# Kernel optimization log

Measured on AMD Instinct MI355X. Metric: run time of the kernel, lower is better.

The kernel has to match this reference:

```python
import jax, jax.numpy as jnp
import numpy as np

D_MODEL = 1024
N_HEADS = 16
HEAD_DIM = D_MODEL // N_HEADS


def setup_inputs() -> dict:
    key = jax.random.key(0)
    ks = jax.random.split(key, 5)
    s = 0.02  # small init scale to keep softmax numerics reasonable
    x = jax.random.normal(ks[0], (4, 2048, D_MODEL), dtype=jnp.float32)
    w_qkv = jax.random.normal(ks[1], (D_MODEL, 3 * D_MODEL), dtype=jnp.float32) * s
    b_qkv = jnp.zeros((3 * D_MODEL,), dtype=jnp.float32)
    w_proj = jax.random.normal(ks[2], (D_MODEL, D_MODEL), dtype=jnp.float32) * s
    b_proj = jnp.zeros((D_MODEL,), dtype=jnp.float32)
    return {"x": x, "w_qkv": w_qkv, "b_qkv": b_qkv, "w_proj": w_proj, "b_proj": b_proj}


def reference(x, w_qkv, b_qkv, w_proj, b_proj):
    B, T, C = x.shape
    scale = 1.0 / np.sqrt(HEAD_DIM)
    qkv = x @ w_qkv + b_qkv                               # [B,T,3C]
    qkv = qkv.reshape(B, T, 3, N_HEADS, HEAD_DIM)
    q = qkv[:, :, 0].transpose(0, 2, 1, 3)               # [B,H,T,D]
    k = qkv[:, :, 1].transpose(0, 2, 1, 3)
    v = qkv[:, :, 2].transpose(0, 2, 1, 3)
    att = jnp.einsum('bhqd,bhkd->bhqk', q, k) * scale    # [B,H,T,T]
    causal = jnp.tril(jnp.ones((T, T), dtype=bool))
    att = jnp.where(causal, att, -jnp.inf)
    att = jax.nn.softmax(att, axis=-1)
    y = jnp.einsum('bhqk,bhkd->bhqd', att, v)            # [B,H,T,D]
    y = y.transpose(0, 2, 1, 3).reshape(B, T, C)
    y = y @ w_proj + b_proj
    return y
```

## Files before the change

### kernel.cpp

```cpp
#include <hip/hip_runtime.h>
#include <stdint.h>

#define BATCH 4
#define SEQ 2048
#define DMODEL 1024
#define NHEADS 16
#define HDIM 64
#define MROWS (BATCH * SEQ)

typedef float floatx4 __attribute__((ext_vector_type(4)));
typedef __bf16 bf16x8 __attribute__((ext_vector_type(8)));
typedef __bf16 bf16x4 __attribute__((ext_vector_type(4)));
typedef short short8 __attribute__((ext_vector_type(8)));

__device__ __forceinline__ unsigned short f32_to_bf16(float f) {
    union { float f; unsigned int u; } c; c.f = f;
    unsigned int u = c.u;
    unsigned int r = (u + 0x7FFFu + ((u >> 16) & 1u)) >> 16;
    return (unsigned short)r;
}

__device__ __forceinline__ void async_ld16(const void* g, void* l) {
    __builtin_amdgcn_global_load_lds(
        (const __attribute__((address_space(1))) unsigned int*)g,
        (__attribute__((address_space(3))) unsigned int*)l, 16, 0, 0);
}

__global__ __launch_bounds__(256) void conv_f32_bf16(
    const float* __restrict__ in, unsigned short* __restrict__ out, int n4) {
    int i = blockIdx.x * 256 + threadIdx.x;
    if (i < n4) {
        float4 v = ((const float4*)in)[i];
        ushort4 o;
        o.x = f32_to_bf16(v.x); o.y = f32_to_bf16(v.y);
        o.z = f32_to_bf16(v.z); o.w = f32_to_bf16(v.w);
        ((ushort4*)out)[i] = o;
    }
}

__global__ __launch_bounds__(256) void transp_conv(
    const float* __restrict__ in, unsigned short* __restrict__ out, int K, int N) {
    __shared__ float tile[32][33];
    int bx = blockIdx.x * 32;
    int by = blockIdx.y * 32;
    int tx = threadIdx.x, ty = threadIdx.y;
#pragma unroll
    for (int i = 0; i < 4; ++i)
        tile[ty + i * 8][tx] = in[(size_t)(by + ty + i * 8) * N + bx + tx];
    __syncthreads();
#pragma unroll
    for (int i = 0; i < 4; ++i)
        out[(size_t)(bx + ty + i * 8) * K + by + tx] = f32_to_bf16(tile[tx][ty + i * 8]);
}

__global__ __launch_bounds__(256) void transp_bf16_head(
    const unsigned short* __restrict__ in, unsigned short* __restrict__ out) {
    __shared__ unsigned short tile[32][33];
    const unsigned short* src = in + (size_t)blockIdx.z * SEQ * HDIM;
    unsigned short* dst = out + (size_t)blockIdx.z * SEQ * HDIM;
    int bx = blockIdx.x * 32;
    int by = blockIdx.y * 32;
    int tx = threadIdx.x, ty = threadIdx.y;
#pragma unroll
    for (int i = 0; i < 4; ++i)
        tile[ty + i * 8][tx] = src[(size_t)(by + ty + i * 8) * HDIM + bx + tx];
    __syncthreads();
#pragma unroll
    for (int i = 0; i < 4; ++i) {
        int keyg = by + tx;
        int col2 = (keyg & ~63) | (((keyg & 15) << 2) | ((keyg >> 4) & 3));
        dst[(size_t)(bx + ty + i * 8) * SEQ + col2] = tile[tx][ty + i * 8];
    }
}

template <int EPI>
__global__ __launch_bounds__(256, 3) void gemm_bt(
    const unsigned short* __restrict__ A, const unsigned short* __restrict__ Bt,
    const float* __restrict__ bias, float* __restrict__ Cout,
    unsigned short* __restrict__ Qo, unsigned short* __restrict__ Ko,
    unsigned short* __restrict__ Vo, int M, int N, int K) {
    __shared__ __align__(16) unsigned short As[3][128 * 32];
    __shared__ __align__(16) unsigned short Bs[3][128 * 32];
    const int tid = threadIdx.x;
    const int lane = tid & 63;
    const int w = tid >> 6;
    const int wm = w & 1, wn = w >> 1;
    const int quad = lane >> 4, l16 = lane & 15;
    const int m0 = blockIdx.y * 128;
    const int n0 = blockIdx.x * 128;
    const int fsw = (l16 >> 1) & 3;

    const int idx0 = tid, idx1 = tid + 256;
    const int row0 = idx0 >> 2, row1 = idx1 >> 2;
    const int cg0 = (idx0 & 3) ^ ((row0 >> 1) & 3);
    const int cg1 = (idx1 & 3) ^ ((row1 >> 1) & 3);
    const unsigned short* Ar0 = &A[(size_t)(m0 + row0) * K + cg0 * 8];
    const unsigned short* Ar1 = &A[(size_t)(m0 + row1) * K + cg1 * 8];
    const unsigned short* Br0 = &Bt[(size_t)(n0 + row0) * K + cg0 * 8];
    const unsigned short* Br1 = &Bt[(size_t)(n0 + row1) * K + cg1 * 8];

    floatx4 acc[4][4];
#pragma unroll
    for (int mt = 0; mt < 4; ++mt)
#pragma unroll
        for (int nt = 0; nt < 4; ++nt) acc[mt][nt] = (floatx4){0.f, 0.f, 0.f, 0.f};

    async_ld16(Ar0, &As[0][idx0 * 8]);
    async_ld16(Br0, &Bs[0][idx0 * 8]);
    async_ld16(Ar1, &As[0][idx1 * 8]);
    async_ld16(Br1, &Bs[0][idx1 * 8]);
    async_ld16(Ar0 + 32, &As[1][idx0 * 8]);
    async_ld16(Br0 + 32, &Bs[1][idx0 * 8]);
    async_ld16(Ar1 + 32, &As[1][idx1 * 8]);
    async_ld16(Br1 + 32, &Bs[1][idx1 * 8]);

    const int nk = K >> 5;
    int bcur = 0, bpre = 2;
    for (int kt = 0; kt < nk; ++kt) {
        if (kt + 2 < nk)
            asm volatile("s_waitcnt vmcnt(4)" ::: "memory");
        else
            asm volatile("s_waitcnt vmcnt(0)" ::: "memory");
        __builtin_amdgcn_s_barrier();
        asm volatile("" ::: "memory");

        if (kt + 2 < nk) {
            const int ko = (kt + 2) << 5;
            async_ld16(Ar0 + ko, &As[bpre][idx0 * 8]);
            async_ld16(Br0 + ko, &Bs[bpre][idx0 * 8]);
            async_ld16(Ar1 + ko, &As[bpre][idx1 * 8]);
            async_ld16(Br1 + ko, &Bs[bpre][idx1 * 8]);
        }

        bf16x8 aF[4], bF[4];
#pragma unroll
        for (int mt = 0; mt < 4; ++mt)
            aF[mt] = *(const bf16x8*)&As[bcur][(wm * 64 + mt * 16 + l16) * 32 + (quad ^ fsw) * 8];
#pragma unroll
        for (int nt = 0; nt < 4; ++nt)
            bF[nt] = *(const bf16x8*)&Bs[bcur][(wn * 64 + nt * 16 + l16) * 32 + (quad ^ fsw) * 8];
#pragma unroll
        for (int mt = 0; mt < 4; ++mt)
#pragma unroll
            for (int nt = 0; nt < 4; ++nt)
                acc[mt][nt] = __builtin_amdgcn_mfma_f32_16x16x32_bf16(
                    aF[mt], bF[nt], acc[mt][nt], 0, 0, 0);

        bcur = (bcur == 2) ? 0 : bcur + 1;
        bpre = (bpre == 2) ? 0 : bpre + 1;
    }

#pragma unroll
    for (int mt = 0; mt < 4; ++mt)
#pragma unroll
        for (int nt = 0; nt < 4; ++nt)
#pragma unroll
            for (int r = 0; r < 4; ++r) {
                int m = m0 + wm * 64 + mt * 16 + quad * 4 + r;
                int n = n0 + wn * 64 + nt * 16 + l16;
                float v = acc[mt][nt][r] + bias[n];
                if (EPI == 1) {
                    Cout[(size_t)m * N + n] = v;
                } else {
                    int sel = n >> 10, c = n & 1023;
                    int head = c >> 6, d = c & 63;
                    int bb = m >> 11, t = m & 2047;
                    unsigned short* dst = sel == 0 ? Qo : (sel == 1 ? Ko : Vo);
                    dst[((((size_t)bb * NHEADS + head) * SEQ + t) << 6) + d] = f32_to_bf16(v);
                }
            }
}

__global__ __launch_bounds__(256, 2) void attn_kernel(
    const unsigned short* __restrict__ Qg, const unsigned short* __restrict__ Kg,
    const unsigned short* __restrict__ Vtg, unsigned short* __restrict__ Yatt) {
    __shared__ __align__(16) unsigned short Kb2[2][4096];
    __shared__ __align__(16) unsigned short Vb2[2][4096];
    __shared__ __align__(16) unsigned short Ps[4][2048];

    const int tid = threadIdx.x;
    const int lane = tid & 63;
    const int w = tid >> 6;
    const int quad = lane >> 4, l16 = lane & 15;
    const int bh = blockIdx.x;
    const int by = blockIdx.y;
    const int sA = by * 4 + w;
    const size_t base = (size_t)bh * SEQ * HDIM;
    const int bIdx = bh >> 4, h = bh & 15;
    unsigned short* Pw = &Ps[w][0];
    const float csc = 0.18033688f;

    const int lrow = lane >> 3;
    const int lch = (lane & 7) ^ lrow;

    short8 osv = {0x3F80, 0x3F80, 0x3F80, 0x3F80, 0x3F80, 0x3F80, 0x3F80, 0x3F80};
    bf16x8 ones = __builtin_bit_cast(bf16x8, osv);

    for (int half = 0; half < 2; ++half) {
        const int rowb = (half == 0 ? sA : 63 - sA) * 32;
        const int kmaxB = (half == 0) ? (2 * by + 2) : (32 - 2 * by);

        bf16x8 qf[2][2];
#pragma unroll
        for (int mt = 0; mt < 2; ++mt)
#pragma unroll
            for (int kk = 0; kk < 2; ++kk)
                qf[mt][kk] = *(const bf16x8*)&Qg[base + (size_t)(rowb + mt * 16 + l16) * 64 +
                                                 kk * 32 + quad * 8];

        floatx4 lsum[2];
        floatx4 o[2][4];
#pragma unroll
        for (int mt = 0; mt < 2; ++mt) {
            lsum[mt] = (floatx4){0.f, 0.f, 0.f, 0.f};
#pragma unroll
            for (int nt = 0; nt < 4; ++nt) o[mt][nt] = (floatx4){0.f, 0.f, 0.f, 0.f};
        }

        {
            const unsigned short* Ktg = Kg + base;
            const unsigned short* Vtg_t = Vtg + base;
#pragma unroll
            for (int ii = 0; ii < 2; ++ii) {
                int i = w * 2 + ii;
                async_ld16(Ktg + (i * 8 + lrow) * 64 + lch * 8,
                           &Kb2[0][i * 512 + lane * 8]);
                async_ld16(Vtg_t + (size_t)(i * 8 + lrow) * SEQ + lch * 8,
                           &Vb2[0][i * 512 + lane * 8]);
            }
        }

        for (int kb = 0; kb < kmaxB; ++kb) {
            const int b = kb & 1;
            __syncthreads();

            if (kb + 1 < kmaxB) {
                const unsigned short* Ktg = Kg + base + (size_t)(kb + 1) * 64 * HDIM;
                const unsigned short* Vtg_t = Vtg + base + (kb + 1) * 64;
#pragma unroll
                for (int ii = 0; ii < 2; ++ii) {
                    int i = w * 2 + ii;
                    async_ld16(Ktg + (i * 8 + lrow) * 64 + lch * 8,
                               &Kb2[1 - b][i * 512 + lane * 8]);
                    async_ld16(Vtg_t + (size_t)(i * 8 + lrow) * SEQ + lch * 8,
                               &Vb2[1 - b][i * 512 + lane * 8]);
                }
            }

            floatx4 s[2][4];
#pragma unroll
            for (int mt = 0; mt < 2; ++mt)
#pragma unroll
                for (int nt = 0; nt < 4; ++nt) s[mt][nt] = (floatx4){0.f, 0.f, 0.f, 0.f};
#pragma unroll
            for (int kk = 0; kk < 2; ++kk) {
                bf16x8 kf[4];
#pragma unroll
                for (int nt = 0; nt < 4; ++nt)
                    kf[nt] = *(const bf16x8*)&Kb2[b][(nt * 16 + l16) * 64 +
                                                     ((kk * 4 + quad) ^ (l16 & 7)) * 8];
#pragma unroll
                for (int nt = 0; nt < 4; ++nt)
#pragma unroll
                    for (int mt = 0; mt < 2; ++mt)
                        s[mt][nt] = __builtin_amdgcn_mfma_f32_16x16x32_bf16(
                            qf[mt][kk], kf[nt], s[mt][nt], 0, 0, 0);
            }

            if ((kb * 64 + 63) > rowb) {
#pragma unroll
                for (int mt = 0; mt < 2; ++mt)
#pragma unroll
                    for (int nt = 0; nt < 4; ++nt)
#pragma unroll
                        for (int r = 0; r < 4; ++r) {
                            int key = kb * 64 + nt * 16 + l16;
                            int qrow = rowb + mt * 16 + quad * 4 + r;
                            if (key > qrow) s[mt][nt][r] = -INFINITY;
                        }
            }

#pragma unroll
            for (int mt = 0; mt < 2; ++mt)
#pragma unroll
                for (int nt = 0; nt < 4; ++nt)
#pragma unroll
                    for (int r = 0; r < 4; ++r)
                        s[mt][nt][r] = __builtin_amdgcn_exp2f(s[mt][nt][r] * csc);

#pragma unroll
            for (int mt = 0; mt < 2; ++mt)
#pragma unroll
                for (int r = 0; r < 4; ++r) {
                    int prow = mt * 16 + quad * 4 + r;
                    int unit = l16 ^ (prow & 14);
                    floatx4 t = {s[mt][0][r], s[mt][1][r], s[mt][2][r], s[mt][3][r]};
                    bf16x4 pv = __builtin_convertvector(t, bf16x4);
                    *(bf16x4*)&Pw[prow * 64 + unit * 4] = pv;
                }

#pragma unroll
            for (int kk = 0; kk < 2; ++kk) {
                bf16x8 af[2];
#pragma unroll
                for (int mt = 0; mt < 2; ++mt) {
                    int prow = mt * 16 + l16;
                    int u2 = (kk * 8 + quad * 2) ^ (l16 & 14);
                    af[mt] = *(const bf16x8*)&Pw[prow * 64 + u2 * 4];
                }
#pragma unroll
                for (int nt = 0; nt < 4; ++nt) {
                    bf16x8 vf = *(const bf16x8*)&Vb2[b][(nt * 16 + l16) * 64 +
                                                        ((kk * 4 + quad) ^ (l16 & 7)) * 8];
#pragma unroll
                    for (int mt = 0; mt < 2; ++mt)
                        o[mt][nt] = __builtin_amdgcn_mfma_f32_16x16x32_bf16(
                            af[mt], vf, o[mt][nt], 0, 0, 0);
                }
#pragma unroll
                for (int mt = 0; mt < 2; ++mt)
                    lsum[mt] = __builtin_amdgcn_mfma_f32_16x16x32_bf16(
                        af[mt], ones, lsum[mt], 0, 0, 0);
            }
        }

#pragma unroll
        for (int mt = 0; mt < 2; ++mt)
#pragma unroll
            for (int r = 0; r < 4; ++r) {
                float inv = 1.0f / lsum[mt][r];
                int qrow = rowb + mt * 16 + quad * 4 + r;
#pragma unroll
                for (int nt = 0; nt < 4; ++nt)
                    Yatt[((size_t)(bIdx * SEQ + qrow) << 10) + h * 64 + nt * 16 + l16] =
                        f32_to_bf16(o[mt][nt][r] * inv);
            }
    }
}

extern "C" void kernel_launch(void* const* d_in, const int* in_sizes, int n_in,
                              void* d_out, int out_size, void* d_ws, size_t ws_size,
                              hipStream_t stream) {
    const float* x = (const float*)d_in[0];
    const float* w_qkv = (const float*)d_in[1];
    const float* b_qkv = (const float*)d_in[2];
    const float* w_proj = (const float*)d_in[3];
    const float* b_proj = (const float*)d_in[4];
    float* out = (float*)d_out;

    char* ws = (char*)d_ws;
    unsigned short* xb     = (unsigned short*)(ws);
    unsigned short* wqkvT  = (unsigned short*)(ws + 16777216);
    unsigned short* wprojT = (unsigned short*)(ws + 23068672);
    unsigned short* Qb     = (unsigned short*)(ws + 25165824);
    unsigned short* Kb     = (unsigned short*)(ws + 41943040);
    unsigned short* Vb     = (unsigned short*)(ws + 58720256);
    unsigned short* Yatt   = (unsigned short*)(ws + 75497472);
    unsigned short* Vt     = (unsigned short*)(ws + 92274688);

    conv_f32_bf16<<<8192, 256, 0, stream>>>(x, xb, (MROWS * DMODEL) / 4);
    transp_conv<<<dim3(96, 32), dim3(32, 8), 0, stream>>>(w_qkv, wqkvT, DMODEL, 3 * DMODEL);
    transp_conv<<<dim3(32, 32), dim3(32, 8), 0, stream>>>(w_proj, wprojT, DMODEL, DMODEL);
    gemm_bt<0><<<dim3(24, 64), 256, 0, stream>>>(xb, wqkvT, b_qkv, nullptr, Qb, Kb, Vb,
                                                 MROWS, 3 * DMODEL, DMODEL);
    transp_bf16_head<<<dim3(2, 64, BATCH * NHEADS), dim3(32, 8), 0, stream>>>(Vb, Vt);
    attn_kernel<<<dim3(64, 8), 256, 0, stream>>>(Qb, Kb, Vt, Yatt);
    gemm_bt<1><<<dim3(8, 64), 256, 0, stream>>>(Yatt, wprojT, b_proj, out, nullptr, nullptr,
                                                nullptr, MROWS, DMODEL, DMODEL);
}
```

Before: 254.0 us.

## Triple-buffer attention K/V loads with vmcnt waits and swizzle GEMM block order

```diff
diff --git a/kernel.cpp b/kernel.cpp
--- a/kernel.cpp
+++ b/kernel.cpp
@@ -86,8 +86,13 @@
     const int w = tid >> 6;
     const int wm = w & 1, wn = w >> 1;
     const int quad = lane >> 4, l16 = lane & 15;
-    const int m0 = blockIdx.y * 128;
-    const int n0 = blockIdx.x * 128;
+
+    const int nbx = gridDim.x;
+    const int nwg = nbx * gridDim.y;
+    const int lin = blockIdx.y * nbx + blockIdx.x;
+    const int swz = (lin & 7) * (nwg >> 3) + (lin >> 3);
+    const int m0 = (swz / nbx) * 128;
+    const int n0 = (swz % nbx) * 128;
     const int fsw = (l16 >> 1) & 3;
 
     const int idx0 = tid, idx1 = tid + 256;
@@ -174,8 +179,8 @@
 __global__ __launch_bounds__(256, 2) void attn_kernel(
     const unsigned short* __restrict__ Qg, const unsigned short* __restrict__ Kg,
     const unsigned short* __restrict__ Vtg, unsigned short* __restrict__ Yatt) {
-    __shared__ __align__(16) unsigned short Kb2[2][4096];
-    __shared__ __align__(16) unsigned short Vb2[2][4096];
+    __shared__ __align__(16) unsigned short Kb2[3][4096];
+    __shared__ __align__(16) unsigned short Vb2[3][4096];
     __shared__ __align__(16) unsigned short Ps[4][2048];
 
     const int tid = threadIdx.x;
@@ -196,6 +201,16 @@
     short8 osv = {0x3F80, 0x3F80, 0x3F80, 0x3F80, 0x3F80, 0x3F80, 0x3F80, 0x3F80};
     bf16x8 ones = __builtin_bit_cast(bf16x8, osv);
 
+    const unsigned short* Ktg = Kg + base;
+    const unsigned short* Vtg_t = Vtg + base;
+    const int i0 = w * 2, i1 = w * 2 + 1;
+    const int kof0 = (i0 * 8 + lrow) * 64 + lch * 8;
+    const int kof1 = (i1 * 8 + lrow) * 64 + lch * 8;
+    const size_t vof0 = (size_t)(i0 * 8 + lrow) * SEQ + lch * 8;
+    const size_t vof1 = (size_t)(i1 * 8 + lrow) * SEQ + lch * 8;
+    const int ld0 = i0 * 512 + lane * 8;
+    const int ld1 = i1 * 512 + lane * 8;
+
     for (int half = 0; half < 2; ++half) {
         const int rowb = (half == 0 ? sA : 63 - sA) * 32;
         const int kmaxB = (half == 0) ? (2 * by + 2) : (32 - 2 * by);
@@ -217,34 +232,31 @@
             for (int nt = 0; nt < 4; ++nt) o[mt][nt] = (floatx4){0.f, 0.f, 0.f, 0.f};
         }
 
-        {
-            const unsigned short* Ktg = Kg + base;
-            const unsigned short* Vtg_t = Vtg + base;
-#pragma unroll
-            for (int ii = 0; ii < 2; ++ii) {
-                int i = w * 2 + ii;
-                async_ld16(Ktg + (i * 8 + lrow) * 64 + lch * 8,
-                           &Kb2[0][i * 512 + lane * 8]);
-                async_ld16(Vtg_t + (size_t)(i * 8 + lrow) * SEQ + lch * 8,
-                           &Vb2[0][i * 512 + lane * 8]);
-            }
-        }
-
+        async_ld16(Ktg + kof0, &Kb2[0][ld0]);
+        async_ld16(Vtg_t + vof0, &Vb2[0][ld0]);
+        async_ld16(Ktg + kof1, &Kb2[0][ld1]);
+        async_ld16(Vtg_t + vof1, &Vb2[0][ld1]);
+        async_ld16(Ktg + 64 * HDIM + kof0, &Kb2[1][ld0]);
+        async_ld16(Vtg_t + 64 + vof0, &Vb2[1][ld0]);
+        async_ld16(Ktg + 64 * HDIM + kof1, &Kb2[1][ld1]);
+        async_ld16(Vtg_t + 64 + vof1, &Vb2[1][ld1]);
+
+        int bcur = 0, bpre = 2;
         for (int kb = 0; kb < kmaxB; ++kb) {
-            const int b = kb & 1;
-            __syncthreads();
-
-            if (kb + 1 < kmaxB) {
-                const unsigned short* Ktg = Kg + base + (size_t)(kb + 1) * 64 * HDIM;
-                const unsigned short* Vtg_t = Vtg + base + (kb + 1) * 64;
-#pragma unroll
-                for (int ii = 0; ii < 2; ++ii) {
-                    int i = w * 2 + ii;
-                    async_ld16(Ktg + (i * 8 + lrow) * 64 + lch * 8,
-                               &Kb2[1 - b][i * 512 + lane * 8]);
-                    async_ld16(Vtg_t + (size_t)(i * 8 + lrow) * SEQ + lch * 8,
-                               &Vb2[1 - b][i * 512 + lane * 8]);
-                }
+            if (kb + 2 < kmaxB)
+                asm volatile("s_waitcnt vmcnt(4)" ::: "memory");
+            else
+                asm volatile("s_waitcnt vmcnt(0)" ::: "memory");
+            __builtin_amdgcn_s_barrier();
+            asm volatile("" ::: "memory");
+
+            if (kb + 2 < kmaxB) {
+                const unsigned short* Kt2 = Ktg + (size_t)(kb + 2) * 64 * HDIM;
+                const unsigned short* Vt2 = Vtg_t + (kb + 2) * 64;
+                async_ld16(Kt2 + kof0, &Kb2[bpre][ld0]);
+                async_ld16(Vt2 + vof0, &Vb2[bpre][ld0]);
+                async_ld16(Kt2 + kof1, &Kb2[bpre][ld1]);
+                async_ld16(Vt2 + vof1, &Vb2[bpre][ld1]);
             }
 
             floatx4 s[2][4];
@@ -257,8 +269,8 @@
                 bf16x8 kf[4];
 #pragma unroll
                 for (int nt = 0; nt < 4; ++nt)
-                    kf[nt] = *(const bf16x8*)&Kb2[b][(nt * 16 + l16) * 64 +
-                                                     ((kk * 4 + quad) ^ (l16 & 7)) * 8];
+                    kf[nt] = *(const bf16x8*)&Kb2[bcur][(nt * 16 + l16) * 64 +
+                                                        ((kk * 4 + quad) ^ (l16 & 7)) * 8];
 #pragma unroll
                 for (int nt = 0; nt < 4; ++nt)
 #pragma unroll
@@ -310,8 +322,8 @@
                 }
 #pragma unroll
                 for (int nt = 0; nt < 4; ++nt) {
-                    bf16x8 vf = *(const bf16x8*)&Vb2[b][(nt * 16 + l16) * 64 +
-                                                        ((kk * 4 + quad) ^ (l16 & 7)) * 8];
+                    bf16x8 vf = *(const bf16x8*)&Vb2[bcur][(nt * 16 + l16) * 64 +
+                                                           ((kk * 4 + quad) ^ (l16 & 7)) * 8];
 #pragma unroll
                     for (int mt = 0; mt < 2; ++mt)
                         o[mt][nt] = __builtin_amdgcn_mfma_f32_16x16x32_bf16(
@@ -322,7 +334,12 @@
                     lsum[mt] = __builtin_amdgcn_mfma_f32_16x16x32_bf16(
                         af[mt], ones, lsum[mt], 0, 0, 0);
             }
+
+            bcur = (bcur == 2) ? 0 : bcur + 1;
+            bpre = (bpre == 2) ? 0 : bpre + 1;
         }
+
+        __syncthreads();
 
 #pragma unroll
         for (int mt = 0; mt < 2; ++mt)
```

New measurement: 253.3 us. About the same (-0.3%).
